# Performance work log

Hardware: AMD Instinct MI355X
Metric: run time of the kernel (lower is better)

Reference implementation:

```python
import jax, jax.numpy as jnp
import numpy as np

DT = 0.02
Z_DIM = 32
U_DIM = 16


def _mlp(x, layers):
    # layers: list of (W, b); SiLU between all but last layer
    n = len(layers)
    for i, (W, b) in enumerate(layers):
        x = x @ W + b
        if i < n - 1:
            x = jax.nn.silu(x)
    return x


def _forward(x, u,
             e_w1, e_b1, e_w2, e_b2, e_w3, e_b3,
             d_w1, d_b1, d_w2, d_b2, d_w3, d_b3, d_w4, d_b4,
             a_w1, a_b1, a_w2, a_b2, a_w3, a_b3,
             b_w1, b_b1, b_w2, b_b2, b_w3, b_b3):
    # encode
    z = _mlp(x, [(e_w1, e_b1), (e_w2, e_b2), (e_w3, e_b3)])          # (B, Z)
    # state-dependent A(x) parameters: pairs (a_i, b_i) per 2x2 block
    aux = _mlp(x, [(a_w1, a_b1), (a_w2, a_b2), (a_w3, a_b3)])        # (B, Z)
    a = aux[:, 0::2]                                                  # (B, Z/2)
    b = aux[:, 1::2]
    f = jnp.exp(a * DT)
    c = jnp.cos(b * DT)
    s = jnp.sin(b * DT)
    # A(x) @ z without materializing block-diagonal: per-pair rotation-scale
    z0 = z[:, 0::2]
    z1 = z[:, 1::2]
    Az = jnp.stack([f * (c * z0 - s * z1), f * (s * z0 + c * z1)], axis=-1).reshape(z.shape)
    # B(x) @ u
    Bmat = _mlp(x, [(b_w1, b_b1), (b_w2, b_b2), (b_w3, b_b3)]).reshape(-1, Z_DIM, U_DIM)
    Bu = jnp.einsum('bzu,bu->bz', Bmat, u)
    # latent Euler step + decode
    z_next = z + DT * (Az + Bu)
    return _mlp(z_next, [(d_w1, d_b1), (d_w2, d_b2), (d_w3, d_b3), (d_w4, d_b4)])


def setup_inputs() -> dict:
    key = jax.random.key(0)
    ks = iter(jax.random.split(key, 32))
    def w(shape, scale=0.02):
        return jax.random.normal(next(ks), shape, jnp.float32) * scale
    B, X, U, Z, H, A = 16384, 64, 16, 32, 1024, 256
    return {
        'x': jax.random.normal(next(ks), (B, X), jnp.float32),
        'u': jax.random.normal(next(ks), (B, U), jnp.float32),
        'e_w1': w((X, H)), 'e_b1': w((H,)),
        'e_w2': w((H, H)), 'e_b2': w((H,)),
        'e_w3': w((H, Z)), 'e_b3': w((Z,)),
        'd_w1': w((Z, H)), 'd_b1': w((H,)),
        'd_w2': w((H, H)), 'd_b2': w((H,)),
        'd_w3': w((H, H)), 'd_b3': w((H,)),
        'd_w4': w((H, X)), 'd_b4': w((X,)),
        'a_w1': w((X, A)), 'a_b1': w((A,)),
        'a_w2': w((A, A)), 'a_b2': w((A,)),
        'a_w3': w((A, Z)), 'a_b3': w((Z,)),
        'b_w1': w((X, A)), 'b_b1': w((A,)),
        'b_w2': w((A, A)), 'b_b2': w((A,)),
        'b_w3': w((A, Z * U)), 'b_b3': w((Z * U,)),
    }


def reference(x, u,
              e_w1, e_b1, e_w2, e_b2, e_w3, e_b3,
              d_w1, d_b1, d_w2, d_b2, d_w3, d_b3, d_w4, d_b4,
              a_w1, a_b1, a_w2, a_b2, a_w3, a_b3,
              b_w1, b_b1, b_w2, b_b2, b_w3, b_b3):
    return _forward(x, u,
                    e_w1, e_b1, e_w2, e_b2, e_w3, e_b3,
                    d_w1, d_b1, d_w2, d_b2, d_w3, d_b3, d_w4, d_b4,
                    a_w1, a_b1, a_w2, a_b2, a_w3, a_b3,
                    b_w1, b_b1, b_w2, b_b2, b_w3, b_b3)
```

## Files before the change

### kernel.cpp

```cpp
#include <hip/hip_runtime.h>
#include <cstdint>
#include <cstddef>

#define B_SZ 16384
#define X_D  64
#define U_D  16
#define Z_D  32
#define H_D  1024
#define A_D  256
#define DT_C 0.02f

typedef _Float16 f16;
typedef f16   f16x8 __attribute__((ext_vector_type(8)));
typedef f16   f16x4 __attribute__((ext_vector_type(4)));
typedef float f32x4 __attribute__((ext_vector_type(4)));
typedef float f32x16 __attribute__((ext_vector_type(16)));

#define AS1 __attribute__((address_space(1)))
#define AS3 __attribute__((address_space(3)))

__device__ __forceinline__ void gld_lds16(const void* g, void* l) {
    __builtin_amdgcn_global_load_lds((AS1 void*)(g), (AS3 void*)(l), 16, 0, 0);
}

#define BARX()  do { asm volatile("" ::: "memory"); __builtin_amdgcn_s_barrier(); \
                     asm volatile("" ::: "memory"); } while (0)
#define LGK0()  do { asm volatile("s_waitcnt lgkmcnt(0)" ::: "memory"); \
                     __builtin_amdgcn_sched_barrier(0); } while (0)
#define WAITV0() asm volatile("s_waitcnt vmcnt(0)" ::: "memory")

struct GArg {
    const f16*  A;
    const f16*  W;
    const float* bias;
    void*       C;
    int lda, ldc, K;
};
struct GSet { GArg g[3]; int yn0, yn1; };

template<int BM,int BN,int BK,int WM,int WN,bool SILU,int OM>
__launch_bounds__(256)
__global__ void gemm_k(GSet p)
{
    static_assert(OM != 1 || BN == 128, "OM1 repack assumes BN=128");
    int yb = blockIdx.y, gi = 0;
    if (yb >= p.yn0) { yb -= p.yn0; gi = 1; if (yb >= p.yn1) { yb -= p.yn1; gi = 2; } }
    const GArg ga = p.g[gi];

    constexpr int SEGROW = BK / 8;
    constexpr int SMASK  = (SEGROW < 8 ? SEGROW : 8) - 1;
    constexpr int WTM = BM / WM, WTN = BN / WN;
    static_assert(WTM % 32 == 0 && WTN % 32 == 0, "wave tile in 32x32 units");
    constexpr int RM = WTM / 32, RN = WTN / 32;
    constexpr int KS = BK / 16;
    constexpr int ITA = (BM * SEGROW) / 256;
    constexpr int ITB = (BN * SEGROW) / 256;

    constexpr int STAGE_B = (BM + BN) * BK * 2;
    constexpr int CS_B    = (OM == 1) ? BM * BN * 2 : 0;
    constexpr int SMEM_B  = STAGE_B > CS_B ? STAGE_B : CS_B;
    __shared__ __align__(16) char smem[SMEM_B];
    f16* As = (f16*)smem;
    f16* Bs = As + BM * BK;

    const int tid  = threadIdx.x;
    const int lane = tid & 63;
    const int wave = tid >> 6;
    const int wm = wave / WN, wn = wave % WN;
    const int l31 = lane & 31, half = lane >> 5;

    const size_t arow0 = (size_t)blockIdx.x * BM;
    const size_t brow0 = (size_t)yb * BN;
    const int lda = ga.lda, K = ga.K;

    const f16* aptr[ITA];
    const f16* bptr[ITB];
#pragma unroll
    for (int it = 0; it < ITA; ++it) {
        int s = it * 256 + tid;
        int row = s / SEGROW, st = s % SEGROW;
        int sg = st ^ (row & SMASK);
        aptr[it] = ga.A + (arow0 + row) * lda + sg * 8;
    }
#pragma unroll
    for (int it = 0; it < ITB; ++it) {
        int s = it * 256 + tid;
        int row = s / SEGROW, st = s % SEGROW;
        int sg = st ^ (row & SMASK);
        bptr[it] = ga.W + (brow0 + row) * K + sg * 8;
    }

    f32x16 acc[RM][RN];
#pragma unroll
    for (int i = 0; i < RM; ++i)
#pragma unroll
        for (int j = 0; j < RN; ++j)
#pragma unroll
            for (int r = 0; r < 16; ++r) acc[i][j][r] = 0.f;

    for (int k0 = 0; k0 < K; k0 += BK) {
#pragma unroll
        for (int it = 0; it < ITA; ++it) {
            gld_lds16(aptr[it], &As[(it * 256 + tid) * 8]);
            aptr[it] += BK;
        }
#pragma unroll
        for (int it = 0; it < ITB; ++it) {
            gld_lds16(bptr[it], &Bs[(it * 256 + tid) * 8]);
            bptr[it] += BK;
        }
        __syncthreads();

#pragma unroll
        for (int ks = 0; ks < KS; ++ks) {
            f16x8 af[RM], bf[RN];
#pragma unroll
            for (int i = 0; i < RM; ++i) {
                int row = wm * WTM + i * 32 + l31;
                int st  = (ks * 2 + half) ^ (row & SMASK);
                af[i] = *(const f16x8*)&As[(row * SEGROW + st) * 8];
            }
#pragma unroll
            for (int j = 0; j < RN; ++j) {
                int row = wn * WTN + j * 32 + l31;
                int st  = (ks * 2 + half) ^ (row & SMASK);
                bf[j] = *(const f16x8*)&Bs[(row * SEGROW + st) * 8];
            }
#pragma unroll
            for (int i = 0; i < RM; ++i)
#pragma unroll
                for (int j = 0; j < RN; ++j)
                    acc[i][j] = __builtin_amdgcn_mfma_f32_32x32x16_f16(
                        af[i], bf[j], acc[i][j], 0, 0, 0);
        }
        __syncthreads();
    }

    const int rowbL = wm * WTM;
    const int colbL = wn * WTN;

    if constexpr (OM == 1) {
        f16* Cs = (f16*)smem;
#pragma unroll
        for (int j = 0; j < RN; ++j) {
            int colL = colbL + j * 32 + l31;
            float bv = ga.bias[(int)brow0 + colL];
            int chL = colL >> 3, wi = colL & 7;
#pragma unroll
            for (int i = 0; i < RM; ++i) {
#pragma unroll
                for (int r = 0; r < 16; ++r) {
                    int rowL = rowbL + i * 32 + (r & 3) + 8 * (r >> 2) + 4 * half;
                    float v = acc[i][j][r] + bv;
                    if (SILU) v = v / (1.0f + __expf(-v));
                    Cs[rowL * BN + ((chL ^ (rowL & 15)) << 3) + wi] = (f16)v;
                }
            }
        }
        __syncthreads();
        f16* Cout = (f16*)ga.C;
#pragma unroll
        for (int pass = 0; pass < (BM * BN / 8) / 256; ++pass) {
            int s = pass * 256 + tid;
            int rowL = s >> 4;
            int ch = s & 15;
            f16x8 v = *(const f16x8*)&Cs[rowL * BN + ((ch ^ (rowL & 15)) << 3)];
            *(f16x8*)&Cout[(size_t)(arow0 + rowL) * ga.ldc + brow0 + ch * 8] = v;
        }
    } else {
        float* Cout = (float*)ga.C;
#pragma unroll
        for (int j = 0; j < RN; ++j) {
            int col = (int)brow0 + colbL + j * 32 + l31;
            float bv = ga.bias[col];
#pragma unroll
            for (int i = 0; i < RM; ++i) {
#pragma unroll
                for (int r = 0; r < 16; ++r) {
                    int row = (int)arow0 + rowbL + i * 32
                            + (r & 3) + 8 * (r >> 2) + 4 * half;
                    float v = acc[i][j][r] + bv;
                    if (SILU) v = v / (1.0f + __expf(-v));
                    Cout[(size_t)row * ga.ldc + col] = v;
                }
            }
        }
    }
}

template<bool SILU>
__launch_bounds__(512, 2)
__global__ void gemm8_k(GSet p)
{
    int yb = blockIdx.y, gi = 0;
    if (yb >= p.yn0) { yb -= p.yn0; gi = 1; if (yb >= p.yn1) { yb -= p.yn1; gi = 2; } }
    const GArg ga = p.g[gi];

    __shared__ __align__(16) char smem[131072];

    const int tid  = threadIdx.x;
    const int lane = tid & 63, wave = tid >> 6;
    const int wm = wave >> 2, wn = wave & 3;
    const int l15 = lane & 15, quad = lane >> 4;
    const int r7  = l15 & 7;

    const size_t arow0 = (size_t)blockIdx.x * 256;
    const size_t brow0 = (size_t)yb * 256;
    const int lda = ga.lda, K = ga.K;
    const int nt = K >> 6;

    const f16* sp[4][2];
#pragma unroll
    for (int q = 0; q < 2; ++q) {
        int s = q * 512 + tid;
        int urow = s >> 3, j = s & 7;
        int kseg = j ^ (urow & 7);
        sp[0][q] = ga.A + (arow0 + urow)       * lda + kseg * 8;
        sp[1][q] = ga.A + (arow0 + 128 + urow) * lda + kseg * 8;
        sp[2][q] = ga.W + (brow0 + urow)       * K   + kseg * 8;
        sp[3][q] = ga.W + (brow0 + 128 + urow) * K   + kseg * 8;
    }

    f32x4 acc[8][4];
#pragma unroll
    for (int i = 0; i < 8; ++i)
#pragma unroll
        for (int j = 0; j < 4; ++j)
#pragma unroll
            for (int r = 0; r < 4; ++r) acc[i][j][r] = 0.f;

    auto stage_u = [&](int u, int bb) {
        char* base = smem + ((u >= 2) ? 65536 : 0)
                   + (size_t)bb * 32768 + (size_t)(u & 1) * 16384;
        gld_lds16(sp[u][0], base + (size_t)tid * 16);         sp[u][0] += 64;
        gld_lds16(sp[u][1], base + (size_t)(512 + tid) * 16); sp[u][1] += 64;
    };

    f16x8 af[4], bf[4];
    auto readA = [&](int b, int ks, int mh) {
        const char* abase = (const char*)smem + (size_t)b * 32768
                          + (size_t)wm * 16384;
        int slot = (((ks << 2) | quad) ^ r7) << 4;
#pragma unroll
        for (int f = 0; f < 4; ++f) {
            int urow = (mh * 4 + f) * 16 + l15;
            af[f] = *(const f16x8*)(abase + urow * 128 + slot);
        }
    };
    auto readB = [&](int b, int ks) {
        const char* bbase = (const char*)smem + 65536 + (size_t)b * 32768
                          + (size_t)(wn >> 1) * 16384;
        int slot = (((ks << 2) | quad) ^ r7) << 4;
#pragma unroll
        for (int f = 0; f < 4; ++f) {
            int urow = (wn & 1) * 64 + f * 16 + l15;
            bf[f] = *(const f16x8*)(bbase + urow * 128 + slot);
        }
    };
    auto mma = [&](int mh) {
        __builtin_amdgcn_s_setprio(1);
#pragma unroll
        for (int f = 0; f < 4; ++f)
#pragma unroll
            for (int n = 0; n < 4; ++n)
                acc[mh * 4 + f][n] = __builtin_amdgcn_mfma_f32_16x16x32_f16(
                    af[f], bf[n], acc[mh * 4 + f][n], 0, 0, 0);
        __builtin_amdgcn_s_setprio(0);
    };

    auto tile = [&](int b, bool dostage) {
        readA(b, 0, 0); readB(b, 0);
        if (dostage) { stage_u(0, b ^ 1); stage_u(2, b ^ 1); }
        BARX(); LGK0(); mma(0); BARX();
        readA(b, 0, 1);
        if (dostage) { stage_u(1, b ^ 1); stage_u(3, b ^ 1); }
        BARX(); LGK0(); mma(1); BARX();
        readA(b, 1, 0); readB(b, 1);
        BARX(); LGK0(); mma(0); BARX();
        readA(b, 1, 1);
        BARX(); LGK0(); mma(1);
        if (dostage) WAITV0();
        BARX();
    };

    stage_u(0, 0); stage_u(2, 0); stage_u(1, 0); stage_u(3, 0);
    WAITV0();
    BARX();

    for (int t = 0; t < nt; ++t)
        tile(t & 1, t + 1 < nt);

    f16* Cs = (f16*)smem;
#pragma unroll
    for (int mf = 0; mf < 8; ++mf)
#pragma unroll
        for (int nf = 0; nf < 4; ++nf) {
            int colL = wn * 64 + nf * 16 + l15;
            float bv = ga.bias[(int)brow0 + colL];
            int ch = colL >> 3, wi = colL & 7;
#pragma unroll
            for (int r = 0; r < 4; ++r) {
                int rowL = wm * 128 + mf * 16 + quad * 4 + r;
                float v = acc[mf][nf][r] + bv;
                if (SILU) v = v / (1.0f + __expf(-v));
                Cs[rowL * 256 + ((ch ^ (rowL & 31)) << 3) + wi] = (f16)v;
            }
        }
    __syncthreads();
    f16* Cout = (f16*)ga.C;
#pragma unroll
    for (int pass = 0; pass < 16; ++pass) {
        int s = pass * 512 + tid;
        int rowL = s >> 5, ch = s & 31;
        f16x8 v = *(const f16x8*)&Cs[rowL * 256 + ((ch ^ (rowL & 31)) << 3)];
        *(f16x8*)&Cout[(size_t)(arow0 + rowL) * ga.ldc + brow0 + ch * 8] = v;
    }
}

__launch_bounds__(256)
__global__ void mid_k(const f16* __restrict__ cc2,
                      const f16* __restrict__ e_w3t, const float* __restrict__ e_b3,
                      const f16* __restrict__ a_w3t, const float* __restrict__ a_b3,
                      const f16* __restrict__ b_w3t, const float* __restrict__ b_b3,
                      const float* __restrict__ u,   f16* __restrict__ znb)
{
    __shared__ __align__(16) f16 As[32 * 64];
    __shared__ __align__(16) f16 Bs[128 * 64];
    __shared__ float zb[32 * 32];
    __shared__ float ab[32 * 32];
    __shared__ float bu[32 * 32];
    __shared__ float ub[32 * 16];

    const int tid  = threadIdx.x;
    const int lane = tid & 63, wave = tid >> 6;
    const int l15 = lane & 15, quad = lane >> 4;
    const int r0 = blockIdx.x * 32;

    ub[tid]       = u[r0 * 16 + tid];
    ub[tid + 256] = u[r0 * 16 + 256 + tid];

#pragma unroll 1
    for (int ph = 0; ph < 2; ++ph) {
        const f16* W    = ph ? a_w3t : e_w3t;
        const float* bs = ph ? a_b3 : e_b3;
        const int K     = ph ? 256 : 1024;
        const int co    = ph ? 1024 : 0;
        float* ob       = ph ? ab : zb;
        f32x4 acc = {0.f, 0.f, 0.f, 0.f};
        for (int k0 = 0; k0 < K; k0 += 64) {
            {
                int row = tid >> 3, sg = (tid & 7) ^ (row & 7);
                gld_lds16(cc2 + (size_t)(r0 + row) * 1536 + co + k0 + sg * 8,
                          &As[tid * 8]);
            }
            {
                int row = tid >> 3, sg = (tid & 7) ^ (row & 7);
                gld_lds16(W + (size_t)row * K + k0 + sg * 8, &Bs[tid * 8]);
            }
            __syncthreads();
#pragma unroll
            for (int kk = 0; kk < 64; kk += 32) {
                int ar = ((wave >> 1) << 4) + l15;
                int ast = ((kk >> 3) + quad) ^ (ar & 7);
                f16x8 af = *(const f16x8*)&As[(ar * 8 + ast) * 8];
                int br = ((wave & 1) << 4) + l15;
                int bst = ((kk >> 3) + quad) ^ (br & 7);
                f16x8 bf = *(const f16x8*)&Bs[(br * 8 + bst) * 8];
                acc = __builtin_amdgcn_mfma_f32_16x16x32_f16(af, bf, acc, 0, 0, 0);
            }
            __syncthreads();
        }
#pragma unroll
        for (int r = 0; r < 4; ++r) {
            int row = ((wave >> 1) << 4) + quad * 4 + r;
            int col = ((wave & 1) << 4) + l15;
            ob[row * 32 + col] = acc[r] + bs[col];
        }
    }

#pragma unroll 1
    for (int ch = 0; ch < 4; ++ch) {
        f32x4 acc[2][2];
#pragma unroll
        for (int i = 0; i < 2; ++i)
#pragma unroll
            for (int j = 0; j < 2; ++j) acc[i][j] = f32x4{0.f, 0.f, 0.f, 0.f};
        for (int k0 = 0; k0 < 256; k0 += 64) {
            {   int row = tid >> 3, sg = (tid & 7) ^ (row & 7);
                gld_lds16(cc2 + (size_t)(r0 + row) * 1536 + 1280 + k0 + sg * 8,
                          &As[tid * 8]);
            }
#pragma unroll
            for (int it = 0; it < 4; ++it) {
                int s = it * 256 + tid;
                int row = s >> 3, sg = (s & 7) ^ (row & 7);
                gld_lds16(b_w3t + (size_t)(ch * 128 + row) * 256 + k0 + sg * 8,
                          &Bs[s * 8]);
            }
            __syncthreads();
#pragma unroll
            for (int kk = 0; kk < 64; kk += 32) {
                f16x8 af[2], bf[2];
#pragma unroll
                for (int i = 0; i < 2; ++i) {
                    int ar = i * 16 + l15;
                    int st = ((kk >> 3) + quad) ^ (ar & 7);
                    af[i] = *(const f16x8*)&As[(ar * 8 + st) * 8];
                }
#pragma unroll
                for (int j = 0; j < 2; ++j) {
                    int br = wave * 32 + j * 16 + l15;
                    int st = ((kk >> 3) + quad) ^ (br & 7);
                    bf[j] = *(const f16x8*)&Bs[(br * 8 + st) * 8];
                }
#pragma unroll
                for (int i = 0; i < 2; ++i)
#pragma unroll
                    for (int j = 0; j < 2; ++j)
                        acc[i][j] = __builtin_amdgcn_mfma_f32_16x16x32_f16(
                            af[i], bf[j], acc[i][j], 0, 0, 0);
            }
            __syncthreads();
        }
#pragma unroll
        for (int j = 0; j < 2; ++j) {
            int colg = ch * 128 + wave * 32 + j * 16 + l15;
            float bv = b_b3[colg];
            int z = colg >> 4;
#pragma unroll
            for (int i = 0; i < 2; ++i) {
#pragma unroll
                for (int r = 0; r < 4; ++r) {
                    int row = i * 16 + quad * 4 + r;
                    float v = (acc[i][j][r] + bv) * ub[row * 16 + l15];
                    v += __shfl_xor(v, 8, 16);
                    v += __shfl_xor(v, 4, 16);
                    v += __shfl_xor(v, 2, 16);
                    v += __shfl_xor(v, 1, 16);
                    if (l15 == 0) bu[row * 32 + z] = v;
                }
            }
        }
    }
    __syncthreads();

#pragma unroll
    for (int t = 0; t < 4; ++t) {
        int idx = t * 256 + tid;
        int row = idx >> 5, z = idx & 31;
        int pb = idx & ~1;
        float a  = ab[pb], b = ab[pb + 1];
        float z0 = zb[pb], z1 = zb[pb + 1];
        float f  = __expf(a * DT_C);
        float c_ = __cosf(b * DT_C);
        float s_ = __sinf(b * DT_C);
        float Az = (z & 1) ? f * (s_ * z0 + c_ * z1) : f * (c_ * z0 - s_ * z1);
        float zc = (z & 1) ? z1 : z0;
        znb[(size_t)(r0 + row) * 32 + z] = (f16)(zc + DT_C * (Az + bu[idx]));
    }
}

struct PrepArgs {
    const float* w[13];
    f16*         wt[13];
    int          K[13];
    int          N[13];
    const float* bsrc[3];
    float*       bias1;
    const float* x;
    f16*         xb;
};

__launch_bounds__(256)
__global__ void prep_k(PrepArgs pa, int ntrans, int ncvt)
{
    int bid = blockIdx.x;
    if (bid < ntrans) {
        int i = 0, t;
        for (;; ++i) {
            t = (pa.K[i] >> 5) * (pa.N[i] >> 5);
            if (bid < t) break;
            bid -= t;
        }
        const int K = pa.K[i], N = pa.N[i];
        const int tn = N >> 5;
        const int k0 = (bid / tn) << 5, n0 = (bid % tn) << 5;
        __shared__ float tbuf[32][33];
        const int tx = threadIdx.x & 31, ty = threadIdx.x >> 5;
        const float* src = pa.w[i];
        f16* dst = pa.wt[i];
#pragma unroll
        for (int r = 0; r < 32; r += 8)
            tbuf[ty + r][tx] = src[(size_t)(k0 + ty + r) * N + n0 + tx];
        __syncthreads();
#pragma unroll
        for (int r = 0; r < 32; r += 8)
            dst[(size_t)(n0 + ty + r) * K + k0 + tx] = (f16)tbuf[tx][ty + r];
    } else if (bid < ntrans + ncvt) {
        int i = ((bid - ntrans) * 256 + threadIdx.x) * 4;
        float4 v = *(const float4*)(pa.x + i);
        f16x4 o = {(f16)v.x, (f16)v.y, (f16)v.z, (f16)v.w};
        *(f16x4*)(pa.xb + i) = o;
    } else {
        int idx = (bid - ntrans - ncvt) * 256 + (int)threadIdx.x;
        float v = (idx < 1024) ? pa.bsrc[0][idx]
                : (idx < 1280) ? pa.bsrc[1][idx - 1024]
                               : pa.bsrc[2][idx - 1280];
        pa.bias1[idx] = v;
    }
}

extern "C" void kernel_launch(void* const* d_in, const int* in_sizes, int n_in,
                              void* d_out, int out_size, void* d_ws, size_t ws_size,
                              hipStream_t stream)
{
    (void)in_sizes; (void)n_in; (void)out_size; (void)ws_size;
    const float* x    = (const float*)d_in[0];
    const float* u    = (const float*)d_in[1];
    const float* e_w1 = (const float*)d_in[2];  const float* e_b1 = (const float*)d_in[3];
    const float* e_w2 = (const float*)d_in[4];  const float* e_b2 = (const float*)d_in[5];
    const float* e_w3 = (const float*)d_in[6];  const float* e_b3 = (const float*)d_in[7];
    const float* d_w1 = (const float*)d_in[8];  const float* d_b1 = (const float*)d_in[9];
    const float* d_w2 = (const float*)d_in[10]; const float* d_b2 = (const float*)d_in[11];
    const float* d_w3 = (const float*)d_in[12]; const float* d_b3 = (const float*)d_in[13];
    const float* d_w4 = (const float*)d_in[14]; const float* d_b4 = (const float*)d_in[15];
    const float* a_w1 = (const float*)d_in[16]; const float* a_b1 = (const float*)d_in[17];
    const float* a_w2 = (const float*)d_in[18]; const float* a_b2 = (const float*)d_in[19];
    const float* a_w3 = (const float*)d_in[20]; const float* a_b3 = (const float*)d_in[21];
    const float* b_w1 = (const float*)d_in[22]; const float* b_b1 = (const float*)d_in[23];
    const float* b_w2 = (const float*)d_in[24]; const float* b_b2 = (const float*)d_in[25];
    const float* b_w3 = (const float*)d_in[26]; const float* b_b3 = (const float*)d_in[27];

    char* p = (char*)d_ws;
    auto alloc = [&](size_t nbytes) -> void* {
        void* r = (void*)p;
        p += (nbytes + 255) & ~(size_t)255;
        return r;
    };
    f16*   xb   = (f16*)  alloc((size_t)B_SZ * X_D * 2);
    f16*   cc1  = (f16*)  alloc((size_t)B_SZ * 1536 * 2);
    f16*   cc2  = (f16*)  alloc((size_t)B_SZ * 1536 * 2);
    f16*   znb  = (f16*)  alloc((size_t)B_SZ * Z_D * 2);
    f16*   h1d  = cc1;
    f16*   h2d  = cc2;
    f16*   h3d  = cc1;
    f16*   W1t   = (f16*)alloc((size_t)1536 * X_D * 2);
    float* bias1 = (float*)alloc(1536 * 4);
    f16* e_w2t = (f16*)alloc((size_t)H_D * H_D * 2);
    f16* e_w3t = (f16*)alloc((size_t)Z_D * H_D * 2);
    f16* d_w1t = (f16*)alloc((size_t)H_D * Z_D * 2);
    f16* d_w2t = (f16*)alloc((size_t)H_D * H_D * 2);
    f16* d_w3t = (f16*)alloc((size_t)H_D * H_D * 2);
    f16* d_w4t = (f16*)alloc((size_t)X_D * H_D * 2);
    f16* a_w2t = (f16*)alloc((size_t)A_D * A_D * 2);
    f16* a_w3t = (f16*)alloc((size_t)Z_D * A_D * 2);
    f16* b_w2t = (f16*)alloc((size_t)A_D * A_D * 2);
    f16* b_w3t = (f16*)alloc((size_t)(Z_D * U_D) * A_D * 2);

    PrepArgs pa;
    const float* ws_[13] = {e_w1, e_w2, e_w3, d_w1, d_w2, d_w3, d_w4,
                            a_w1, a_w2, a_w3, b_w1, b_w2, b_w3};
    f16* wts_[13] = {W1t, e_w2t, e_w3t, d_w1t, d_w2t, d_w3t, d_w4t,
                     W1t + (size_t)1024 * X_D, a_w2t, a_w3t,
                     W1t + (size_t)1280 * X_D, b_w2t, b_w3t};
    int Ks_[13] = {X_D, H_D, H_D, Z_D, H_D, H_D, H_D, X_D, A_D, A_D, X_D, A_D, A_D};
    int Ns_[13] = {H_D, H_D, Z_D, H_D, H_D, H_D, X_D, A_D, A_D, Z_D, A_D, A_D, Z_D*U_D};
    int ntrans = 0;
    for (int i = 0; i < 13; ++i) {
        pa.w[i] = ws_[i]; pa.wt[i] = wts_[i]; pa.K[i] = Ks_[i]; pa.N[i] = Ns_[i];
        ntrans += (Ks_[i] >> 5) * (Ns_[i] >> 5);
    }
    pa.bsrc[0] = e_b1; pa.bsrc[1] = a_b1; pa.bsrc[2] = b_b1;
    pa.bias1 = bias1; pa.x = x; pa.xb = xb;
    const int ncvt = (B_SZ * X_D) / 1024;
    prep_k<<<ntrans + ncvt + 6, 256, 0, stream>>>(pa, ntrans, ncvt);

    auto G = [](const f16* A, const f16* W, const float* bias, void* C,
                int lda, int ldc, int K) {
        GArg g; g.A = A; g.W = W; g.bias = bias; g.C = C;
        g.lda = lda; g.ldc = ldc; g.K = K; return g;
    };
    GSet s;

    s.g[0] = G(xb, W1t, bias1, cc1, X_D, 1536, X_D);
    s.yn0 = 12; s.yn1 = 0;
    gemm_k<128,128,64,2,2,true,1><<<dim3(B_SZ/128, 12), 256, 0, stream>>>(s);

    s.g[0] = G(cc1,        e_w2t, e_b2, cc2,        1536, 1536, H_D);
    s.g[1] = G(cc1 + 1024, a_w2t, a_b2, cc2 + 1024, 1536, 1536, A_D);
    s.g[2] = G(cc1 + 1280, b_w2t, b_b2, cc2 + 1280, 1536, 1536, A_D);
    s.yn0 = 4; s.yn1 = 1;
    gemm8_k<true><<<dim3(B_SZ/256, 6), 512, 0, stream>>>(s);

    mid_k<<<B_SZ/32, 256, 0, stream>>>(cc2, e_w3t, e_b3, a_w3t, a_b3,
                                       b_w3t, b_b3, u, znb);

    s.yn0 = 8; s.yn1 = 0;
    s.g[0] = G(znb, d_w1t, d_b1, h1d, Z_D, H_D, Z_D);
    gemm_k<128,128,32,2,2,true,1><<<dim3(B_SZ/128, 8), 256, 0, stream>>>(s);

    s.yn0 = 4; s.yn1 = 0;
    s.g[0] = G(h1d, d_w2t, d_b2, h2d, H_D, H_D, H_D);
    gemm8_k<true><<<dim3(B_SZ/256, 4), 512, 0, stream>>>(s);

    s.g[0] = G(h2d, d_w3t, d_b3, h3d, H_D, H_D, H_D);
    gemm8_k<true><<<dim3(B_SZ/256, 4), 512, 0, stream>>>(s);

    s.g[0] = G(h3d, d_w4t, d_b4, d_out, H_D, X_D, H_D);
    s.yn0 = 1;
    gemm_k<64,64,64,2,2,false,0><<<dim3(B_SZ/64, 1), 256, 0, stream>>>(s);
}
```

Measured before the change: 352.2 us.

## Halve GEMM row tile and add triple-buffered LDS prefetch pipeline

Replaces the 256x256 double-buffered big GEMM kernel with a 128x256 tile kernel that uses three LDS stages, prefetching two K-tiles ahead and waiting with a partial vmcnt instead of draining all loads. The smaller M tile doubles the grid size, which gives more blocks to spread across CUs. The deeper pipeline is meant to hide global-to-LDS latency. In exchange, each block reuses weight tiles over fewer rows, raising B-operand traffic, and LDS use rises to 144KB per block, which limits co-residency.

```diff
diff --git a/kernel.cpp b/kernel.cpp
--- a/kernel.cpp
+++ b/kernel.cpp
@@ -27,6 +27,7 @@
                      asm volatile("" ::: "memory"); } while (0)
 #define LGK0()  do { asm volatile("s_waitcnt lgkmcnt(0)" ::: "memory"); \
                      __builtin_amdgcn_sched_barrier(0); } while (0)
+#define WAITV6() asm volatile("s_waitcnt vmcnt(6)" ::: "memory")
 #define WAITV0() asm volatile("s_waitcnt vmcnt(0)" ::: "memory")
 
 struct GArg {
@@ -190,13 +191,13 @@
 
 template<bool SILU>
 __launch_bounds__(512, 2)
-__global__ void gemm8_k(GSet p)
+__global__ void gemm9_k(GSet p)
 {
     int yb = blockIdx.y, gi = 0;
     if (yb >= p.yn0) { yb -= p.yn0; gi = 1; if (yb >= p.yn1) { yb -= p.yn1; gi = 2; } }
     const GArg ga = p.g[gi];
 
-    __shared__ __align__(16) char smem[131072];
+    __shared__ __align__(16) char smem[147456];
 
     const int tid  = threadIdx.x;
     const int lane = tid & 63, wave = tid >> 6;
@@ -204,95 +205,108 @@
     const int l15 = lane & 15, quad = lane >> 4;
     const int r7  = l15 & 7;
 
-    const size_t arow0 = (size_t)blockIdx.x * 256;
+    const size_t arow0 = (size_t)blockIdx.x * 128;
     const size_t brow0 = (size_t)yb * 256;
     const int lda = ga.lda, K = ga.K;
     const int nt = K >> 6;
 
-    const f16* sp[4][2];
+    const f16* spA[2];
+    const f16* spB[4];
 #pragma unroll
     for (int q = 0; q < 2; ++q) {
         int s = q * 512 + tid;
-        int urow = s >> 3, j = s & 7;
-        int kseg = j ^ (urow & 7);
-        sp[0][q] = ga.A + (arow0 + urow)       * lda + kseg * 8;
-        sp[1][q] = ga.A + (arow0 + 128 + urow) * lda + kseg * 8;
-        sp[2][q] = ga.W + (brow0 + urow)       * K   + kseg * 8;
-        sp[3][q] = ga.W + (brow0 + 128 + urow) * K   + kseg * 8;
-    }
-
-    f32x4 acc[8][4];
-#pragma unroll
-    for (int i = 0; i < 8; ++i)
+        int urow = s >> 3;
+        int kseg = (s & 7) ^ (urow & 7);
+        spA[q] = ga.A + (arow0 + urow) * lda + kseg * 8;
+    }
+#pragma unroll
+    for (int q = 0; q < 4; ++q) {
+        int s = q * 512 + tid;
+        int urow = s >> 3;
+        int kseg = (s & 7) ^ (urow & 7);
+        spB[q] = ga.W + (brow0 + urow) * K + kseg * 8;
+    }
+
+    f32x4 acc[4][4];
+#pragma unroll
+    for (int i = 0; i < 4; ++i)
 #pragma unroll
         for (int j = 0; j < 4; ++j)
 #pragma unroll
             for (int r = 0; r < 4; ++r) acc[i][j][r] = 0.f;
 
-    auto stage_u = [&](int u, int bb) {
-        char* base = smem + ((u >= 2) ? 65536 : 0)
-                   + (size_t)bb * 32768 + (size_t)(u & 1) * 16384;
-        gld_lds16(sp[u][0], base + (size_t)tid * 16);         sp[u][0] += 64;
-        gld_lds16(sp[u][1], base + (size_t)(512 + tid) * 16); sp[u][1] += 64;
+    auto stageA = [&](char* buf, int q) {
+        gld_lds16(spA[q], buf + (size_t)(q * 512 + tid) * 16);
+        spA[q] += 64;
     };
-
-    f16x8 af[4], bf[4];
-    auto readA = [&](int b, int ks, int mh) {
-        const char* abase = (const char*)smem + (size_t)b * 32768
-                          + (size_t)wm * 16384;
-        int slot = (((ks << 2) | quad) ^ r7) << 4;
+    auto stageB = [&](char* buf, int q) {
+        gld_lds16(spB[q], buf + 16384 + (size_t)(q * 512 + tid) * 16);
+        spB[q] += 64;
+    };
+
+    f16x8 af[2], bf[4];
+    auto readA = [&](const char* buf, int ks, int mh) {
+        int slot = ((ks << 2) | quad) ^ r7;
+#pragma unroll
+        for (int f = 0; f < 2; ++f) {
+            int row = wm * 64 + mh * 32 + f * 16 + l15;
+            af[f] = *(const f16x8*)(buf + row * 128 + slot * 16);
+        }
+    };
+    auto readB = [&](const char* buf, int ks) {
+        int slot = ((ks << 2) | quad) ^ r7;
 #pragma unroll
         for (int f = 0; f < 4; ++f) {
-            int urow = (mh * 4 + f) * 16 + l15;
-            af[f] = *(const f16x8*)(abase + urow * 128 + slot);
-        }
-    };
-    auto readB = [&](int b, int ks) {
-        const char* bbase = (const char*)smem + 65536 + (size_t)b * 32768
-                          + (size_t)(wn >> 1) * 16384;
-        int slot = (((ks << 2) | quad) ^ r7) << 4;
-#pragma unroll
-        for (int f = 0; f < 4; ++f) {
-            int urow = (wn & 1) * 64 + f * 16 + l15;
-            bf[f] = *(const f16x8*)(bbase + urow * 128 + slot);
+            int row = wn * 64 + f * 16 + l15;
+            bf[f] = *(const f16x8*)(buf + 16384 + row * 128 + slot * 16);
         }
     };
     auto mma = [&](int mh) {
         __builtin_amdgcn_s_setprio(1);
 #pragma unroll
-        for (int f = 0; f < 4; ++f)
+        for (int f = 0; f < 2; ++f)
 #pragma unroll
             for (int n = 0; n < 4; ++n)
-                acc[mh * 4 + f][n] = __builtin_amdgcn_mfma_f32_16x16x32_f16(
-                    af[f], bf[n], acc[mh * 4 + f][n], 0, 0, 0);
+                acc[mh * 2 + f][n] = __builtin_amdgcn_mfma_f32_16x16x32_f16(
+                    af[f], bf[n], acc[mh * 2 + f][n], 0, 0, 0);
         __builtin_amdgcn_s_setprio(0);
     };
 
-    auto tile = [&](int b, bool dostage) {
-        readA(b, 0, 0); readB(b, 0);
-        if (dostage) { stage_u(0, b ^ 1); stage_u(2, b ^ 1); }
+    {
+        char* b0 = smem;
+        char* b1 = smem + 49152;
+        stageB(b0, 0); stageB(b0, 1); stageB(b0, 2); stageB(b0, 3);
+        stageA(b0, 0); stageA(b0, 1);
+        stageB(b1, 0); stageB(b1, 1); stageB(b1, 2); stageB(b1, 3);
+        stageA(b1, 0); stageA(b1, 1);
+        WAITV6();
+        BARX();
+    }
+
+    int bi = 0;
+    for (int t = 0; t < nt; ++t) {
+        char* buf = smem + bi * 49152;
+        int nxi = bi + 2; if (nxi >= 3) nxi -= 3;
+        char* nbuf = smem + nxi * 49152;
+        const bool st = (t + 2 < nt);
+        readA(buf, 0, 0); readB(buf, 0);
+        if (st) { stageB(nbuf, 0); stageB(nbuf, 1); }
         BARX(); LGK0(); mma(0); BARX();
-        readA(b, 0, 1);
-        if (dostage) { stage_u(1, b ^ 1); stage_u(3, b ^ 1); }
+        readA(buf, 0, 1);
+        if (st) { stageB(nbuf, 2); stageB(nbuf, 3); }
         BARX(); LGK0(); mma(1); BARX();
-        readA(b, 1, 0); readB(b, 1);
+        readA(buf, 1, 0); readB(buf, 1);
+        if (st) { stageA(nbuf, 0); stageA(nbuf, 1); }
         BARX(); LGK0(); mma(0); BARX();
-        readA(b, 1, 1);
-        BARX(); LGK0(); mma(1);
-        if (dostage) WAITV0();
-        BARX();
-    };
-
-    stage_u(0, 0); stage_u(2, 0); stage_u(1, 0); stage_u(3, 0);
-    WAITV0();
-    BARX();
-
-    for (int t = 0; t < nt; ++t)
-        tile(t & 1, t + 1 < nt);
+        readA(buf, 1, 1);
+        if (st) WAITV6(); else if (t + 1 < nt) WAITV0();
+        BARX(); LGK0(); mma(1); BARX();
+        bi += 1; if (bi >= 3) bi -= 3;
+    }
 
     f16* Cs = (f16*)smem;
 #pragma unroll
-    for (int mf = 0; mf < 8; ++mf)
+    for (int mf = 0; mf < 4; ++mf)
 #pragma unroll
         for (int nf = 0; nf < 4; ++nf) {
             int colL = wn * 64 + nf * 16 + l15;
@@ -300,7 +314,7 @@
             int ch = colL >> 3, wi = colL & 7;
 #pragma unroll
             for (int r = 0; r < 4; ++r) {
-                int rowL = wm * 128 + mf * 16 + quad * 4 + r;
+                int rowL = wm * 64 + (mf >> 1) * 32 + (mf & 1) * 16 + quad * 4 + r;
                 float v = acc[mf][nf][r] + bv;
                 if (SILU) v = v / (1.0f + __expf(-v));
                 Cs[rowL * 256 + ((ch ^ (rowL & 31)) << 3) + wi] = (f16)v;
@@ -309,7 +323,7 @@
     __syncthreads();
     f16* Cout = (f16*)ga.C;
 #pragma unroll
-    for (int pass = 0; pass < 16; ++pass) {
+    for (int pass = 0; pass < 8; ++pass) {
         int s = pass * 512 + tid;
         int rowL = s >> 5, ch = s & 31;
         f16x8 v = *(const f16x8*)&Cs[rowL * 256 + ((ch ^ (rowL & 31)) << 3)];
@@ -590,7 +604,7 @@
     s.g[1] = G(cc1 + 1024, a_w2t, a_b2, cc2 + 1024, 1536, 1536, A_D);
     s.g[2] = G(cc1 + 1280, b_w2t, b_b2, cc2 + 1280, 1536, 1536, A_D);
     s.yn0 = 4; s.yn1 = 1;
-    gemm8_k<true><<<dim3(B_SZ/256, 6), 512, 0, stream>>>(s);
+    gemm9_k<true><<<dim3(B_SZ/128, 6), 512, 0, stream>>>(s);
 
     mid_k<<<B_SZ/32, 256, 0, stream>>>(cc2, e_w3t, e_b3, a_w3t, a_b3,
                                        b_w3t, b_b3, u, znb);
@@ -601,10 +615,10 @@
 
     s.yn0 = 4; s.yn1 = 0;
     s.g[0] = G(h1d, d_w2t, d_b2, h2d, H_D, H_D, H_D);
-    gemm8_k<true><<<dim3(B_SZ/256, 4), 512, 0, stream>>>(s);
+    gemm9_k<true><<<dim3(B_SZ/128, 4), 512, 0, stream>>>(s);
 
     s.g[0] = G(h2d, d_w3t, d_b3, h3d, H_D, H_D, H_D);
-    gemm8_k<true><<<dim3(B_SZ/256, 4), 512, 0, stream>>>(s);
+    gemm9_k<true><<<dim3(B_SZ/128, 4), 512, 0, stream>>>(s);
 
     s.g[0] = G(h3d, d_w4t, d_b4, d_out, H_D, X_D, H_D);
     s.yn0 = 1;
```

Result: slower. 361.7 us (+2.7%).
